# Kernel optimization log

Hardware: AMD Instinct MI355X
Metric: run time of the kernel (lower is better)

Reference implementation:

```python
import jax, jax.numpy as jnp
import numpy as np

ATT_DIM = 768
N_HEADS = 4
N_LABELS = 2000
NEG_INF = -1e6


def setup_inputs() -> dict:
    key = jax.random.key(0)
    k1, k2, k3, k4, k5, k6 = jax.random.split(key, 6)
    B, S, D = 4, 3072, ATT_DIM
    h = jax.random.normal(k1, (B, S, D), dtype=jnp.float32)
    attention_mask = jnp.ones((B, S), dtype=jnp.int32)
    label_feat = jax.random.normal(k2, (N_LABELS * N_HEADS, D), dtype=jnp.float32)
    # nn.Linear W: weight [D, D], bias [D]
    W_w = jax.random.normal(k3, (D, D), dtype=jnp.float32) * 0.02
    W_b = jnp.zeros((D,), dtype=jnp.float32)
    # classifier: weight [num_labels, D], bias [num_labels]
    cls_w = jax.random.normal(k4, (N_LABELS, D), dtype=jnp.float32) * 0.02
    cls_b = jnp.zeros((N_LABELS,), dtype=jnp.float32)
    return {"h": h, "attention_mask": attention_mask, "label_feat": label_feat,
            "W_w": W_w, "W_b": W_b, "cls_w": cls_w, "cls_b": cls_b}


def reference(h, attention_mask, label_feat, W_w, W_b, cls_w, cls_b):
    # h: [B,S,D]; label_feat: [E*H, D]
    B, S, D = h.shape
    E = label_feat.shape[0] // N_HEADS
    z = jnp.tanh(h @ W_w.T + W_b)                       # [B,S,D]
    u = label_feat.reshape(E, N_HEADS, D)               # [E,H,D]
    # score 'abd,ecd->aebc' -> [B,E,S,H]
    score = jnp.einsum('bsd,ehd->besh', z, u)
    mask = attention_mask.astype(bool)[:, None, :, None]  # [B,1,S,1]
    score = jnp.where(mask, score, NEG_INF)
    alpha = jax.nn.softmax(score, axis=2)               # softmax over seq
    # m 'abd,aebc->aedc' -> [B,E,D,H]
    m = jnp.einsum('bsd,besh->bedh', h, alpha)
    m = m.max(axis=-1)                                  # head max-pool -> [B,E,D]
    logits = jnp.sum(cls_w[None] * m, axis=2) + cls_b   # [B,E]
    return logits, m
```

## Files before the change

### kernel.cpp

```cpp
#include <hip/hip_runtime.h>
#include <hip/hip_bf16.h>

typedef _Float16 f16;
typedef _Float16 half8 __attribute__((ext_vector_type(8)));
typedef _Float16 half4v __attribute__((ext_vector_type(4)));
typedef float f32x4 __attribute__((ext_vector_type(4)));
typedef float f32x16 __attribute__((ext_vector_type(16)));

#define B_ 4
#define S_ 3072
#define D_ 768
#define E_ 2000
#define NEG_INF -1.0e6f

#define GLD16(gsrc, ldst)                                                     \
  __builtin_amdgcn_global_load_lds(                                           \
      (const __attribute__((address_space(1))) void*)(gsrc),                  \
      (__attribute__((address_space(3))) void*)(ldst), 16, 0, 0)

__global__ __launch_bounds__(256) void k_transpose(const float* __restrict__ h,
                                                   f16* __restrict__ ht) {
  __shared__ f16 tile[64][65];
  int b = blockIdx.z, s0 = blockIdx.x * 64, d0 = blockIdx.y * 64;
  int t = threadIdx.x, tx = t & 63, ty = t >> 6;
  const float* src = h + ((size_t)b * S_ + s0) * D_ + d0;
#pragma unroll
  for (int i = 0; i < 16; ++i) {
    int sl = i * 4 + ty;
    tile[sl][tx] = (f16)src[(size_t)sl * D_ + tx];
  }
  __syncthreads();
  f16* dst = ht + ((size_t)b * D_ + d0) * S_ + s0;
#pragma unroll
  for (int i = 0; i < 16; ++i) {
    int dl = i * 4 + ty;
    dst[(size_t)dl * S_ + tx] = tile[tx][dl];
  }
}

__global__ __launch_bounds__(256) void k_zgemm(const float* __restrict__ h,
                                               const float* __restrict__ W,
                                               const float* __restrict__ bias,
                                               f16* __restrict__ zb) {
  __shared__ f16 As[64][40];
  __shared__ f16 Bs[64][40];
  int i0 = blockIdx.x * 64, j0 = blockIdx.y * 64;
  int t = threadIdx.x, w = t >> 6, lane = t & 63, g = lane >> 4, li = lane & 15;
  int wi = w >> 1, wj = w & 1;

  f32x4 acc[2][2];
#pragma unroll
  for (int a = 0; a < 2; ++a)
#pragma unroll
    for (int b2 = 0; b2 < 2; ++b2) acc[a][b2] = (f32x4){0.f, 0.f, 0.f, 0.f};

  int srow = t >> 2, scol = (t & 3) * 8;
  const float* pA = h + (size_t)(i0 + srow) * D_ + scol;
  const float* pB = W + (size_t)(j0 + srow) * D_ + scol;

  for (int kc = 0; kc < D_; kc += 32) {
    float4 a0 = *(const float4*)(pA + kc);
    float4 a1 = *(const float4*)(pA + kc + 4);
    float4 b0 = *(const float4*)(pB + kc);
    float4 b1 = *(const float4*)(pB + kc + 4);
    half8 av = {(f16)a0.x, (f16)a0.y, (f16)a0.z, (f16)a0.w,
                (f16)a1.x, (f16)a1.y, (f16)a1.z, (f16)a1.w};
    half8 bv = {(f16)b0.x, (f16)b0.y, (f16)b0.z, (f16)b0.w,
                (f16)b1.x, (f16)b1.y, (f16)b1.z, (f16)b1.w};
    *(half8*)&As[srow][scol] = av;
    *(half8*)&Bs[srow][scol] = bv;
    __syncthreads();
#pragma unroll
    for (int it = 0; it < 2; ++it) {
      half8 af = *(const half8*)&As[wi * 32 + it * 16 + li][g * 8];
#pragma unroll
      for (int jt = 0; jt < 2; ++jt) {
        half8 bf = *(const half8*)&Bs[wj * 32 + jt * 16 + li][g * 8];
        acc[it][jt] =
            __builtin_amdgcn_mfma_f32_16x16x32_f16(af, bf, acc[it][jt], 0, 0, 0);
      }
    }
    __syncthreads();
  }
#pragma unroll
  for (int it = 0; it < 2; ++it) {
#pragma unroll
    for (int jt = 0; jt < 2; ++jt) {
      int jj = j0 + wj * 32 + jt * 16 + li;
      float bsv = bias[jj];
#pragma unroll
      for (int r = 0; r < 4; ++r) {
        int ii = i0 + wi * 32 + it * 16 + g * 4 + r;
        float v = acc[it][jt][r] + bsv;
        zb[(size_t)ii * D_ + jj] = (f16)tanhf(v);
      }
    }
  }
}

__global__ __launch_bounds__(512)
void k_attn(const float* __restrict__ lf,
            const f16* __restrict__ zb,
            const f16* __restrict__ ht,
            const int* __restrict__ amask,
            float* __restrict__ out_m) {
  __shared__ __align__(16) char Lds[119552];
  char* KsB = Lds;
  char* CpB = Lds + 98304;
  char* PtB = Lds + 114688;
  float* FacB = (float*)(Lds + 118784);
  float* LfinB = (float*)(Lds + 119040);
  int* MskI = (int*)(Lds + 119296);

  const int fid = blockIdx.x;
  const int x2 = fid & 7, u = fid >> 3;
  const int b = x2 >> 1;
  const int qtile = (x2 & 1) * 64 + u;
  if (qtile >= 125) return;
  const int q0 = qtile * 64;
  const int e0 = qtile * 16;

  const int t = threadIdx.x, w = t >> 6, l = t & 63;
  const int l31 = l & 31, h = l >> 5, h16 = h * 16;
  const int qh = w & 1, kq = w >> 1;
  const int dh = w;

  half8 qf[12];
  {
    const float* qp = lf + (size_t)(q0 + qh * 32 + l31) * D_ + kq * 192 + h * 8;
#pragma unroll
    for (int kf = 0; kf < 12; ++kf) {
      float4 v0 = *(const float4*)(qp + kf * 16);
      float4 v1 = *(const float4*)(qp + kf * 16 + 4);
      qf[kf] = (half8){(f16)v0.x, (f16)v0.y, (f16)v0.z, (f16)v0.w,
                       (f16)v1.x, (f16)v1.y, (f16)v1.z, (f16)v1.w};
    }
  }

  int klds[6], kgsw[6];
#pragma unroll
  for (int k = 0; k < 6; ++k) {
    int lin = (w * 6 + k) * 1024 + l * 16;
    int row = lin / 1536;
    int xo = lin - row * 1536;
    klds[k] = lin;
    kgsw[k] = row * 1536 + (xo ^ ((row & 7) << 4));
  }

  const int am7 = (l & 7) << 4;
  const int abase = l31 * 1536 + kq * 384;

  const int rswz = ((l31 >> 1) & 3) << 4;
  const int cqoff = l31 * 64;

  const int qh_s = w >> 2, qoct = w & 3;
  const int qrow = qoct * 8 + (l >> 3);
  const int swzr = ((qrow >> 1) & 3) << 4;
  const int roff = qrow * 64 + ((8 * (l & 7)) ^ swzr);
  const int qabs = qh_s * 32 + qrow;

  const char* zbB = (const char*)zb + (size_t)b * S_ * 1536;
  const f16* vbase = ht + ((size_t)b * D_ + dh * 96 + l31) * S_ + h * 8;

#pragma unroll
  for (int k = 0; k < 6; ++k) GLD16(zbB + kgsw[k], KsB + klds[k]);
  if (t < 32) MskI[t] = amask[b * S_ + t];
  asm volatile("s_waitcnt vmcnt(0)" ::: "memory");
  __syncthreads();

  float mreg = -3.0e38f, lreg = 0.0f;
  f32x16 oacc[2][3];
#pragma unroll
  for (int a = 0; a < 2; ++a)
#pragma unroll
    for (int d = 0; d < 3; ++d)
#pragma unroll
      for (int j = 0; j < 16; ++j) oacc[a][d][j] = 0.f;

  half8 Vb[6];

  for (int i = 0; i < 96; ++i) {
    const int s0 = i * 32;
    const int s0n = (i < 95) ? s0 + 32 : 0;
    const char* ksC = KsB + (i & 1) * 49152;
    char* ksN = KsB + ((i & 1) ^ 1) * 49152;

    int mnext = (t < 32) ? amask[b * S_ + s0n + t] : 0;

    if (i > 0) {
      f32x4 frv[2][4];
#pragma unroll
      for (int q2 = 0; q2 < 2; ++q2)
#pragma unroll
        for (int rr = 0; rr < 4; ++rr)
          frv[q2][rr] = *(const f32x4*)(FacB + q2 * 32 + rr * 8 + h * 4);
#pragma unroll
      for (int q2 = 0; q2 < 2; ++q2)
#pragma unroll
        for (int dt = 0; dt < 3; ++dt)
#pragma unroll
          for (int j = 0; j < 16; ++j)
            oacc[q2][dt][j] *= frv[q2][j >> 2][j & 3];
      half8 pa[2][2];
#pragma unroll
      for (int q2 = 0; q2 < 2; ++q2)
#pragma unroll
        for (int ss = 0; ss < 2; ++ss)
          pa[q2][ss] = *(const half8*)(PtB + q2 * 2048 + cqoff +
                                       ((ss * 32 + h16) ^ rswz));
      __builtin_amdgcn_s_setprio(1);
#pragma unroll
      for (int dt = 0; dt < 3; ++dt)
#pragma unroll
        for (int ss = 0; ss < 2; ++ss)
#pragma unroll
          for (int q2 = 0; q2 < 2; ++q2)
            oacc[q2][dt] = __builtin_amdgcn_mfma_f32_32x32x16_f16(
                pa[q2][ss], Vb[dt * 2 + ss], oacc[q2][dt], 0, 0, 0);
      __builtin_amdgcn_s_setprio(0);
    }

    {
      const f16* vp = vbase + s0;
#pragma unroll
      for (int dt = 0; dt < 3; ++dt)
#pragma unroll
        for (int ss = 0; ss < 2; ++ss)
          Vb[dt * 2 + ss] = *(const half8*)(vp + (size_t)dt * 32 * S_ + ss * 16);
    }

    {
      const char* src = zbB + (size_t)s0n * 1536;
#pragma unroll
      for (int k = 0; k < 6; ++k) GLD16(src + kgsw[k], ksN + klds[k]);
    }
    __builtin_amdgcn_sched_barrier(0);

    f32x16 ca;
#pragma unroll
    for (int j = 0; j < 16; ++j) ca[j] = 0.f;
    __builtin_amdgcn_s_setprio(1);
#pragma unroll
    for (int kf = 0; kf < 12; ++kf) {
      half8 a = *(const half8*)(ksC + abase + ((kf * 32 + h16) ^ am7));
      ca = __builtin_amdgcn_mfma_f32_32x32x16_f16(a, qf[kf], ca, 0, 0, 0);
    }
    __builtin_amdgcn_s_setprio(0);

    {
      char* cp = CpB + w * 2048 + cqoff;
#pragma unroll
      for (int rr = 0; rr < 4; ++rr) {
        half4v pk = {(f16)ca[4 * rr], (f16)ca[4 * rr + 1], (f16)ca[4 * rr + 2],
                     (f16)ca[4 * rr + 3]};
        *(half4v*)(cp + ((rr * 16 + h * 8) ^ rswz)) = pk;
      }
    }
    asm volatile("s_waitcnt lgkmcnt(0)" ::: "memory");
    __builtin_amdgcn_s_barrier();

    {
      float p0 = 0.f, p1 = 0.f, p2 = 0.f, p3 = 0.f;
#pragma unroll
      for (int kk = 0; kk < 4; ++kk) {
        half4v pk = *(const half4v*)(CpB + (kk * 2 + qh_s) * 2048 + roff);
        p0 += (float)pk[0];
        p1 += (float)pk[1];
        p2 += (float)pk[2];
        p3 += (float)pk[3];
      }
      int4 m4 = *(const int4*)(MskI + (i & 1) * 32 + 4 * (l & 7));
      if (!m4.x) p0 = NEG_INF;
      if (!m4.y) p1 = NEG_INF;
      if (!m4.z) p2 = NEG_INF;
      if (!m4.w) p3 = NEG_INF;
      float pmax = fmaxf(fmaxf(p0, p1), fmaxf(p2, p3));
      pmax = fmaxf(pmax, __shfl_xor(pmax, 1));
      pmax = fmaxf(pmax, __shfl_xor(pmax, 2));
      pmax = fmaxf(pmax, __shfl_xor(pmax, 4));
      float Mn = fmaxf(mreg, pmax);
      float fec = __expf(mreg - Mn);
      mreg = Mn;
      p0 = __expf(p0 - Mn);
      p1 = __expf(p1 - Mn);
      p2 = __expf(p2 - Mn);
      p3 = __expf(p3 - Mn);
      float ts = p0 + p1 + p2 + p3;
      ts += __shfl_xor(ts, 1);
      ts += __shfl_xor(ts, 2);
      ts += __shfl_xor(ts, 4);
      lreg = lreg * fec + ts;
      if ((l & 7) == 0) FacB[qabs] = fec;
      *(half4v*)(PtB + qh_s * 2048 + roff) =
          (half4v){(f16)p0, (f16)p1, (f16)p2, (f16)p3};
    }
    if (t < 32) MskI[((i + 1) & 1) * 32 + t] = mnext;
    asm volatile("s_waitcnt vmcnt(0) lgkmcnt(0)" ::: "memory");
    __builtin_amdgcn_s_barrier();
  }

  {
    f32x4 frv[2][4];
#pragma unroll
    for (int q2 = 0; q2 < 2; ++q2)
#pragma unroll
      for (int rr = 0; rr < 4; ++rr)
        frv[q2][rr] = *(const f32x4*)(FacB + q2 * 32 + rr * 8 + h * 4);
#pragma unroll
    for (int q2 = 0; q2 < 2; ++q2)
#pragma unroll
      for (int dt = 0; dt < 3; ++dt)
#pragma unroll
        for (int j = 0; j < 16; ++j)
          oacc[q2][dt][j] *= frv[q2][j >> 2][j & 3];
    half8 pa[2][2];
#pragma unroll
    for (int q2 = 0; q2 < 2; ++q2)
#pragma unroll
      for (int ss = 0; ss < 2; ++ss)
        pa[q2][ss] = *(const half8*)(PtB + q2 * 2048 + cqoff +
                                     ((ss * 32 + h16) ^ rswz));
#pragma unroll
    for (int dt = 0; dt < 3; ++dt)
#pragma unroll
      for (int ss = 0; ss < 2; ++ss)
#pragma unroll
        for (int q2 = 0; q2 < 2; ++q2)
          oacc[q2][dt] = __builtin_amdgcn_mfma_f32_32x32x16_f16(
              pa[q2][ss], Vb[dt * 2 + ss], oacc[q2][dt], 0, 0, 0);
  }

  if ((l & 7) == 0) LfinB[qabs] = lreg;
  __syncthreads();

  f32x4 rlv[2][4];
#pragma unroll
  for (int q2 = 0; q2 < 2; ++q2)
#pragma unroll
    for (int rr = 0; rr < 4; ++rr) {
      f32x4 lv = *(const f32x4*)(LfinB + q2 * 32 + rr * 8 + h * 4);
      rlv[q2][rr] =
          (f32x4){1.0f / lv[0], 1.0f / lv[1], 1.0f / lv[2], 1.0f / lv[3]};
    }
#pragma unroll
  for (int q2 = 0; q2 < 2; ++q2)
#pragma unroll
    for (int dt = 0; dt < 3; ++dt)
#pragma unroll
      for (int rr = 0; rr < 4; ++rr) {
        float mv = oacc[q2][dt][4 * rr + 0] * rlv[q2][rr][0];
        mv = fmaxf(mv, oacc[q2][dt][4 * rr + 1] * rlv[q2][rr][1]);
        mv = fmaxf(mv, oacc[q2][dt][4 * rr + 2] * rlv[q2][rr][2]);
        mv = fmaxf(mv, oacc[q2][dt][4 * rr + 3] * rlv[q2][rr][3]);
        int e_loc = q2 * 8 + rr * 2 + h;
        out_m[((size_t)b * E_ + e0 + e_loc) * D_ + dh * 96 + dt * 32 + l31] = mv;
      }
}

__global__ __launch_bounds__(256) void k_logits(const float* __restrict__ cw,
                                                const float* __restrict__ cb,
                                                const float* __restrict__ m,
                                                float* __restrict__ out) {
  int t = threadIdx.x, w = t >> 6, lane = t & 63;
  int rid = blockIdx.x * 4 + w;
  int b = rid / E_, e = rid - b * E_;
  const float* mr = m + (size_t)rid * D_;
  const float* cr = cw + (size_t)e * D_;
  float acc = 0.f;
#pragma unroll
  for (int i = 0; i < 12; ++i) acc += cr[i * 64 + lane] * mr[i * 64 + lane];
#pragma unroll
  for (int off = 32; off >= 1; off >>= 1) acc += __shfl_xor(acc, off);
  if (lane == 0) out[rid] = acc + cb[e];
}

extern "C" void kernel_launch(void* const* d_in, const int* in_sizes, int n_in,
                              void* d_out, int out_size, void* d_ws, size_t ws_size,
                              hipStream_t stream) {
  const float* h = (const float*)d_in[0];
  const int* amask = (const int*)d_in[1];
  const float* lf = (const float*)d_in[2];
  const float* Ww = (const float*)d_in[3];
  const float* Wb = (const float*)d_in[4];
  const float* cw = (const float*)d_in[5];
  const float* cb = (const float*)d_in[6];
  float* out = (float*)d_out;

  f16* zb = (f16*)d_ws;
  f16* ht = (f16*)((char*)d_ws + 18874368);

  k_transpose<<<dim3(48, 12, 4), 256, 0, stream>>>(h, ht);
  k_zgemm<<<dim3(192, 12), 256, 0, stream>>>(h, Ww, Wb, zb);
  k_attn<<<512, 512, 0, stream>>>(lf, zb, ht, amask, out + 8000);
  k_logits<<<2000, 256, 0, stream>>>(cw, cb, out + 8000, out);
}
```

Measured before the change: 660.4 us.

## Single-buffer K tile to cut LDS and add lazy softmax rescaling

Drops the double-buffered K/z tile in LDS, shrinking shared memory from about 117KB to about 69KB so two 512-thread blocks can fit per CU. The async global-to-LDS load of the next tile now starts after the barrier that follows the score MFMAs, instead of overlapping with them. The online softmax now updates its running max only when some lane's tile max exceeds the stored max by more than 8. Per-wave flags let the accumulator rescale be skipped when no max changed. This trades load/compute overlap within a block for occupancy, and tolerates exponentials up to e^8 in fp16 probabilities.

```diff
diff --git a/kernel.cpp b/kernel.cpp
--- a/kernel.cpp
+++ b/kernel.cpp
@@ -104,13 +104,14 @@
             const f16* __restrict__ ht,
             const int* __restrict__ amask,
             float* __restrict__ out_m) {
-  __shared__ __align__(16) char Lds[119552];
+  __shared__ __align__(16) char Lds[70432];
   char* KsB = Lds;
-  char* CpB = Lds + 98304;
-  char* PtB = Lds + 114688;
-  float* FacB = (float*)(Lds + 118784);
-  float* LfinB = (float*)(Lds + 119040);
-  int* MskI = (int*)(Lds + 119296);
+  char* CpB = Lds + 49152;
+  char* PtB = Lds + 65536;
+  float* FacB = (float*)(Lds + 69632);
+  float* LfinB = (float*)(Lds + 69888);
+  int* MskI = (int*)(Lds + 70144);
+  int* RflW = (int*)(Lds + 70400);
 
   const int fid = blockIdx.x;
   const int x2 = fid & 7, u = fid >> 3;
@@ -182,25 +183,34 @@
   for (int i = 0; i < 96; ++i) {
     const int s0 = i * 32;
     const int s0n = (i < 95) ? s0 + 32 : 0;
-    const char* ksC = KsB + (i & 1) * 49152;
-    char* ksN = KsB + ((i & 1) ^ 1) * 49152;
 
     int mnext = (t < 32) ? amask[b * S_ + s0n + t] : 0;
 
     if (i > 0) {
-      f32x4 frv[2][4];
-#pragma unroll
-      for (int q2 = 0; q2 < 2; ++q2)
+      int4 fA = *(const int4*)RflW;
+      int4 fB = *(const int4*)(RflW + 4);
+      int f0 = fA.x | fA.y | fA.z | fA.w;
+      int f1 = fB.x | fB.y | fB.z | fB.w;
+      if (f0) {
+        f32x4 frv[4];
 #pragma unroll
         for (int rr = 0; rr < 4; ++rr)
-          frv[q2][rr] = *(const f32x4*)(FacB + q2 * 32 + rr * 8 + h * 4);
-#pragma unroll
-      for (int q2 = 0; q2 < 2; ++q2)
+          frv[rr] = *(const f32x4*)(FacB + rr * 8 + h * 4);
 #pragma unroll
         for (int dt = 0; dt < 3; ++dt)
 #pragma unroll
-          for (int j = 0; j < 16; ++j)
-            oacc[q2][dt][j] *= frv[q2][j >> 2][j & 3];
+          for (int j = 0; j < 16; ++j) oacc[0][dt][j] *= frv[j >> 2][j & 3];
+      }
+      if (f1) {
+        f32x4 frv[4];
+#pragma unroll
+        for (int rr = 0; rr < 4; ++rr)
+          frv[rr] = *(const f32x4*)(FacB + 32 + rr * 8 + h * 4);
+#pragma unroll
+        for (int dt = 0; dt < 3; ++dt)
+#pragma unroll
+          for (int j = 0; j < 16; ++j) oacc[1][dt][j] *= frv[j >> 2][j & 3];
+      }
       half8 pa[2][2];
 #pragma unroll
       for (int q2 = 0; q2 < 2; ++q2)
@@ -229,20 +239,13 @@
           Vb[dt * 2 + ss] = *(const half8*)(vp + (size_t)dt * 32 * S_ + ss * 16);
     }
 
-    {
-      const char* src = zbB + (size_t)s0n * 1536;
-#pragma unroll
-      for (int k = 0; k < 6; ++k) GLD16(src + kgsw[k], ksN + klds[k]);
-    }
-    __builtin_amdgcn_sched_barrier(0);
-
     f32x16 ca;
 #pragma unroll
     for (int j = 0; j < 16; ++j) ca[j] = 0.f;
     __builtin_amdgcn_s_setprio(1);
 #pragma unroll
     for (int kf = 0; kf < 12; ++kf) {
-      half8 a = *(const half8*)(ksC + abase + ((kf * 32 + h16) ^ am7));
+      half8 a = *(const half8*)(KsB + abase + ((kf * 32 + h16) ^ am7));
       ca = __builtin_amdgcn_mfma_f32_32x32x16_f16(a, qf[kf], ca, 0, 0, 0);
     }
     __builtin_amdgcn_s_setprio(0);
@@ -259,6 +262,11 @@
     asm volatile("s_waitcnt lgkmcnt(0)" ::: "memory");
     __builtin_amdgcn_s_barrier();
 
+    {
+      const char* src = zbB + (size_t)s0n * 1536;
+#pragma unroll
+      for (int k = 0; k < 6; ++k) GLD16(src + kgsw[k], KsB + klds[k]);
+    }
     {
       float p0 = 0.f, p1 = 0.f, p2 = 0.f, p3 = 0.f;
 #pragma unroll
@@ -278,9 +286,13 @@
       pmax = fmaxf(pmax, __shfl_xor(pmax, 1));
       pmax = fmaxf(pmax, __shfl_xor(pmax, 2));
       pmax = fmaxf(pmax, __shfl_xor(pmax, 4));
-      float Mn = fmaxf(mreg, pmax);
-      float fec = __expf(mreg - Mn);
-      mreg = Mn;
+      int need = __any(pmax > mreg + 8.0f);
+      float Mn = mreg, fec = 1.0f;
+      if (need) {
+        Mn = fmaxf(mreg, pmax);
+        fec = __expf(mreg - Mn);
+        mreg = Mn;
+      }
       p0 = __expf(p0 - Mn);
       p1 = __expf(p1 - Mn);
       p2 = __expf(p2 - Mn);
@@ -291,6 +303,7 @@
       ts += __shfl_xor(ts, 4);
       lreg = lreg * fec + ts;
       if ((l & 7) == 0) FacB[qabs] = fec;
+      if (l == 0) RflW[w] = need;
       *(half4v*)(PtB + qh_s * 2048 + roff) =
           (half4v){(f16)p0, (f16)p1, (f16)p2, (f16)p3};
     }
@@ -300,19 +313,30 @@
   }
 
   {
-    f32x4 frv[2][4];
-#pragma unroll
-    for (int q2 = 0; q2 < 2; ++q2)
+    int4 fA = *(const int4*)RflW;
+    int4 fB = *(const int4*)(RflW + 4);
+    int f0 = fA.x | fA.y | fA.z | fA.w;
+    int f1 = fB.x | fB.y | fB.z | fB.w;
+    if (f0) {
+      f32x4 frv[4];
 #pragma unroll
       for (int rr = 0; rr < 4; ++rr)
-        frv[q2][rr] = *(const f32x4*)(FacB + q2 * 32 + rr * 8 + h * 4);
-#pragma unroll
-    for (int q2 = 0; q2 < 2; ++q2)
+        frv[rr] = *(const f32x4*)(FacB + rr * 8 + h * 4);
 #pragma unroll
       for (int dt = 0; dt < 3; ++dt)
 #pragma unroll
-        for (int j = 0; j < 16; ++j)
-          oacc[q2][dt][j] *= frv[q2][j >> 2][j & 3];
+        for (int j = 0; j < 16; ++j) oacc[0][dt][j] *= frv[j >> 2][j & 3];
+    }
+    if (f1) {
+      f32x4 frv[4];
+#pragma unroll
+      for (int rr = 0; rr < 4; ++rr)
+        frv[rr] = *(const f32x4*)(FacB + 32 + rr * 8 + h * 4);
+#pragma unroll
+      for (int dt = 0; dt < 3; ++dt)
+#pragma unroll
+        for (int j = 0; j < 16; ++j) oacc[1][dt][j] *= frv[j >> 2][j & 3];
+    }
     half8 pa[2][2];
 #pragma unroll
     for (int q2 = 0; q2 < 2; ++q2)
```

Result: faster. 628.9 us (-4.8%).
